# Kernel optimization log

Hardware: AMD Instinct MI355X
Metric: run time of the kernel (lower is better)

The kernel has to match this reference:

```python
import jax, jax.numpy as jnp
import numpy as np

NUT_GAIN = -0.99      # inverting nut reflection
BRIDGE_GAIN = -0.99   # inverting bridge reflection (with one-zero lowpass damping)
VIBRATE_GAIN = 0.999  # per-round-trip mute/loss gain
DISP_A = 0.7          # dispersion filter FIR blend coefficient


def _shift1(x):
    # one-sample delay along time axis: y[t] = x[t-1], y[0] = 0
    return jnp.pad(x, ((0, 0), (1, 0)))[:, :-1]


def _frac_delay(x, d):
    # fractional delay of d samples via linear interpolation: y[t] = x[t - d]
    T = x.shape[-1]
    pos = jnp.arange(T, dtype=jnp.float32) - d  # [T]
    i0 = jnp.floor(pos).astype(jnp.int32)
    f = (pos - i0).astype(x.dtype)

    def take(i):
        v = x[:, jnp.clip(i, 0, T - 1)]  # gather along time, broadcast over batch
        return jnp.where(i >= 0, v, jnp.zeros_like(v))

    return (1.0 - f) * take(i0) + f * take(i0 + 1)


def setup_inputs() -> dict:
    key = jax.random.key(0)
    k1, k2 = jax.random.split(key)
    B, T = 64, 32000  # batch_size=64, seconds=2.0 at SR=16000
    return {
        "length": 128,
        "pluckPosition": jax.random.uniform(k1, (1,), dtype=jnp.float32),
        "excitation": jax.random.normal(k2, (B, T), dtype=jnp.float32),
    }


def reference(length, pluckPosition, excitation):
    T = excitation.shape[-1]
    n_loops = T // int(length)  # matches excitation.size(-1) // int(length.min())
    p = 0.1 + 0.8 * pluckPosition[0]  # keep both string segments non-degenerate
    nUp = length * p           # nut-side segment delay (samples)
    nDown = length * (1.0 - p)  # bridge-side segment delay (samples)

    # chain._start: inject excitation into both traveling waves
    l0 = 0.5 * excitation
    r0 = 0.5 * excitation

    def step(carry, _):
        l, r, ls, rs = carry
        # _lterminate: left-going wave travels nUp to the nut and reflects
        r_next = (NUT_GAIN * VIBRATE_GAIN) * _frac_delay(l, nUp)
        # _rterminate: right-going wave through dispersion filter, nDown to bridge,
        # reflects through one-zero lowpass damping
        disp_r = DISP_A * r + (1.0 - DISP_A) * _shift1(r)
        b_in = _frac_delay(disp_r, nDown)
        l_next = (BRIDGE_GAIN * VIBRATE_GAIN * 0.5) * (b_in + _shift1(b_in))
        return (l_next, r_next, ls + l_next, rs + r_next), None

    (_, _, ls, rs), _ = jax.lax.scan(step, (l0, r0, l0, r0), None, length=n_loops)
    # torch code sums left_signal / right_signal stacks over the loop dim
    return (ls, rs)
```

## Files before the change

### kernel.cpp

```cpp
#include <hip/hip_runtime.h>


#define TLEN   32000
#define NROW   64
#define CHUNK  8000
#define NTH    1024
#define PT     16
#define PT4    (PT/4)
#define SPAN   (NTH*PT)
#define HALO   (SPAN-CHUNK)
#define PADF   1056
#define BUF    (PADF+SPAN)

__device__ inline int swz4(int f) {
  int B = f >> 2;
  B ^= (B >> 3) & 7;
  return B << 2;
}

__device__ inline float sgprf(float x) {
  return __uint_as_float(__builtin_amdgcn_readfirstlane(__float_as_uint(x)));
}

struct Cf { int DU, DD, QB; float a[2], b[4], q[5], q2[9], q4[17], q8[33]; };

__device__ inline void build_from(float Lf, float pv, Cf& c) {
  const float p   = 0.1f + 0.8f * pv;
  const float nUp = Lf * p;
  const float nDn = Lf * (1.0f - p);
  c.DU = (int)ceilf(nUp);
  c.DD = (int)ceilf(nDn);
  const float fU = (float)c.DU - nUp;
  const float fD = (float)c.DD - nDn;
  const float GN  = -0.99f * 0.999f;
  const float GB2 = -0.99f * 0.999f * 0.5f;
  c.a[0] = GN * (1.0f - fU);
  c.a[1] = GN * fU;
  const float w0 = 1.0f - fD, w1 = fD;
  c.b[0] = GB2 * (0.3f * w0);
  c.b[1] = GB2 * (w0 + 0.3f * w1);
  c.b[2] = GB2 * (0.7f * w0 + w1);
  c.b[3] = GB2 * (0.7f * w1);
  c.QB = c.DU + c.DD + 2;
#pragma unroll
  for (int m = 0; m < 5; ++m) c.q[m] = 0.f;
#pragma unroll
  for (int i = 0; i < 2; ++i)
#pragma unroll
    for (int j = 0; j < 4; ++j) c.q[i+j] = fmaf(c.a[i], c.b[j], c.q[i+j]);
#pragma unroll
  for (int m = 0; m < 9; ++m) c.q2[m] = 0.f;
#pragma unroll
  for (int i = 0; i < 5; ++i)
#pragma unroll
    for (int j = 0; j < 5; ++j) c.q2[i+j] = fmaf(c.q[i], c.q[j], c.q2[i+j]);
#pragma unroll
  for (int m = 0; m < 17; ++m) c.q4[m] = 0.f;
#pragma unroll
  for (int i = 0; i < 9; ++i)
#pragma unroll
    for (int j = 0; j < 9; ++j) c.q4[i+j] = fmaf(c.q2[i], c.q2[j], c.q4[i+j]);
#pragma unroll
  for (int m = 0; m < 33; ++m) c.q8[m] = 0.f;
#pragma unroll
  for (int i = 0; i < 17; ++i)
#pragma unroll
    for (int j = 0; j < 17; ++j) c.q8[i+j] = fmaf(c.q4[i], c.q4[j], c.q8[i+j]);
}

template<int NF4>
__device__ inline void ldwin(const float* b, int basef, float* v) {
#pragma unroll
  for (int i = 0; i < NF4; ++i) {
    float4 t4 = *(const float4*)&b[swz4(basef + 4*i)];
    v[4*i+0] = t4.x; v[4*i+1] = t4.y; v[4*i+2] = t4.z; v[4*i+3] = t4.w;
  }
}

__device__ inline void stown(float* b, const int* wro, const float* v) {
#pragma unroll
  for (int k = 0; k < PT4; ++k)
    *(float4*)&b[wro[k]] = make_float4(v[4*k], v[4*k+1], v[4*k+2], v[4*k+3]);
}

__global__ __launch_bounds__(NTH, 4)
void gs_pass(const int* __restrict__ lenp, const float* __restrict__ pp,
             const float* __restrict__ exc,
             float* __restrict__ zg, float* __restrict__ sg,
             float* __restrict__ lout, float* __restrict__ rout, int pass)
{
  __shared__ __align__(16) float bufA[BUF];
  __shared__ __align__(16) float bufB[BUF];

  const int row   = blockIdx.x >> 2;
  const int chunk = blockIdx.x & 3;
  const int t0    = chunk * CHUNK;
  const int tid   = threadIdx.x;
  const int sbase = tid * PT;
  const size_t rb = (size_t)row * TLEN;
  const int steps = pass ? 7 : 8;

  int E8;
  float W[33];
  {
    Cf c0; build_from((float)lenp[0], pp[0], c0);
#pragma unroll
    for (int m = 0; m < 33; ++m) W[m] = sgprf(c0.q8[m]);
    E8 = 8 * c0.QB;
  }

  int rdo[12], wro[PT4];
#pragma unroll
  for (int i = 0; i < 12; ++i) rdo[i] = swz4(PADF + sbase - E8 + 4*i);
#pragma unroll
  for (int k = 0; k < PT4; ++k) wro[k] = swz4(PADF + sbase + 4*k);

  const float4 f4z = make_float4(0.f, 0.f, 0.f, 0.f);
  if (tid * 4 < PADF) {
    *(float4*)&bufA[swz4(tid*4)] = f4z;
    *(float4*)&bufB[swz4(tid*4)] = f4z;
  }
  if (chunk == 0) {
    for (int s4 = tid*4; s4 < HALO; s4 += NTH*4)
      *(float4*)&bufB[swz4(PADF + s4)] = f4z;
  }
#pragma unroll
  for (int k = 0; k < 4; ++k) {
    int s4 = tid*4 + k*(NTH*4);
    int t  = t0 - HALO + s4;
    float4 v = f4z;
    if (t >= 0) {
      if (pass == 0) {
        float4 e = *(const float4*)&exc[rb + t];
        v = make_float4(0.5f*e.x, 0.5f*e.y, 0.5f*e.z, 0.5f*e.w);
      } else {
        v = *(const float4*)&zg[rb + t];
      }
    }
    *(float4*)&bufA[swz4(PADF + s4)] = v;
  }
  __syncthreads();

  float* cur = bufA;
  float* nxt = bufB;

  float z[PT], acc[PT];
#pragma unroll
  for (int k = 0; k < PT4; ++k) {
    float4 t4 = *(const float4*)&cur[wro[k]];
    z[4*k+0] = t4.x; z[4*k+1] = t4.y; z[4*k+2] = t4.z; z[4*k+3] = t4.w;
  }
#pragma unroll
  for (int j = 0; j < PT; ++j) acc[j] = 0.f;

  for (int s = 0; s < steps; ++s) {
    const int limit = (chunk == 0) ? HALO : (s + 1) * E8;
    const bool alive = (sbase + PT > limit);
    if (alive) {
      float v[48];
#pragma unroll
      for (int i = 0; i < 12; ++i) {
        float4 t4 = *(const float4*)&cur[rdo[i]];
        v[4*i+0] = t4.x; v[4*i+1] = t4.y; v[4*i+2] = t4.z; v[4*i+3] = t4.w;
      }
#pragma unroll
      for (int j = 0; j < PT; ++j) acc[j] += z[j];
#pragma unroll
      for (int j = 0; j < PT; ++j) {
        float sv = W[0] * v[j];
#pragma unroll
        for (int m = 1; m < 33; ++m) sv = fmaf(W[m], v[j+m], sv);
        z[j] = sv;
      }
      stown(nxt, wro, z);
    }
    __syncthreads();
    float* tp = cur; cur = nxt; nxt = tp;
  }

  if (pass == 0) {
    stown(nxt, wro, acc);
    __syncthreads();
#pragma unroll
    for (int k = 0; k < 2; ++k) {
      int s4 = HALO + tid*4 + k*(NTH*4);
      if (s4 < SPAN) {
        int t = t0 + s4 - HALO;
        *(float4*)&zg[rb + t] = *(const float4*)&cur[swz4(PADF + s4)];
        *(float4*)&sg[rb + t] = *(const float4*)&nxt[swz4(PADF + s4)];
      }
    }
    return;
  }

  stown(nxt, wro, acc);
  __syncthreads();
#pragma unroll
  for (int k = 0; k < 4; ++k) {
    int s4 = tid*4 + k*(NTH*4);
    int t  = t0 - HALO + s4;
    float4 sv = f4z;
    if (t >= 0) sv = *(const float4*)&sg[rb + t];
    int o = swz4(PADF + s4);
    float4 a4 = *(const float4*)&nxt[o];
    *(float4*)&nxt[o] = make_float4(a4.x + sv.x, a4.y + sv.y,
                                    a4.z + sv.z, a4.w + sv.w);
  }
  __syncthreads();

  Cf c;
  {
    volatile const int* vl = lenp;
    volatile const float* vp = pp;
    build_from((float)vl[0], vp[0], c);
  }
  const int L2 = 2*c.QB, L4 = 4*c.QB, LQ = c.QB, LB = c.DD + 2, LA = c.DU;
  const int L2e = (L2+3)&~3, sh2 = L2e-L2;
  const int LQe = (LQ+3)&~3, shq = LQe-LQ;
  const int LBe = (LB+3)&~3, shb = LBe-LB;
  const int LAe = (LA+3)&~3, sha = LAe-LA;
  float q4f[17], T2[12], TQ[8], TB[7], TA[5];
#pragma unroll
  for (int i = 0; i < 17; ++i) q4f[i] = sgprf(c.q4[i]);
#pragma unroll
  for (int m = 0; m < 12; ++m) {
    float v = 0.f;
#pragma unroll
    for (int i = 0; i < 9; ++i) if (m == sh2 + i) v = c.q2[i];
    T2[m] = sgprf(v);
  }
#pragma unroll
  for (int m = 0; m < 8; ++m) {
    float v = 0.f;
#pragma unroll
    for (int i = 0; i < 5; ++i) if (m == shq + i) v = c.q[i];
    TQ[m] = sgprf(v);
  }
#pragma unroll
  for (int m = 0; m < 7; ++m) {
    float v = 0.f;
#pragma unroll
    for (int i = 0; i < 4; ++i) if (m == shb + i) v = c.b[i];
    TB[m] = sgprf(v);
  }
#pragma unroll
  for (int m = 0; m < 5; ++m) {
    float v = 0.f;
#pragma unroll
    for (int i = 0; i < 2; ++i) if (m == sha + i) v = c.a[i];
    TA[m] = sgprf(v);
  }

  const int  F0 = 7 * E8;
  const bool ae = (chunk == 0) || (sbase + PT > F0);

  float H1[PT], Y2[PT], z62[PT];
  if (ae) {
    float e0[PT];
#pragma unroll
    for (int k = 0; k < PT4; ++k) {
      float4 t4 = *(const float4*)&nxt[wro[k]];
      e0[4*k+0] = t4.x; e0[4*k+1] = t4.y; e0[4*k+2] = t4.z; e0[4*k+3] = t4.w;
    }
    float w[28];
    ldwin<7>(nxt, PADF + sbase - L2e, w);
#pragma unroll
    for (int j = 0; j < PT; ++j) {
      float sv = e0[j];
#pragma unroll
      for (int m = 0; m < 12; ++m) sv = fmaf(T2[m], w[j+m], sv);
      H1[j] = sv;
    }
    ldwin<7>(cur, PADF + sbase - L2e, w);
#pragma unroll
    for (int j = 0; j < PT; ++j) {
      float sv = z[j];
#pragma unroll
      for (int m = 0; m < 12; ++m) sv = fmaf(T2[m], w[j+m], sv);
      Y2[j] = sv;
    }
    float w4[32];
    ldwin<8>(cur, PADF + sbase - L4, w4);
#pragma unroll
    for (int j = 0; j < PT; ++j) {
      float sv = q4f[0] * w4[j];
#pragma unroll
      for (int m = 1; m < 17; ++m) sv = fmaf(q4f[m], w4[j+m], sv);
      z62[j] = sv;
    }
  }
  __syncthreads();
  if (ae) { stown(nxt, wro, H1); stown(cur, wro, z62); }
  __syncthreads();

  float E61[PT];
  if (ae) {
    float w4[32];
    ldwin<8>(nxt, PADF + sbase - L4, w4);
#pragma unroll
    for (int j = 0; j < PT; ++j) {
      float sv = H1[j] + Y2[j];
#pragma unroll
      for (int m = 0; m < 17; ++m) sv = fmaf(q4f[m], w4[j+m], sv);
      E61[j] = sv;
    }
  }
  __syncthreads();
  if (ae) stown(nxt, wro, E61);
  __syncthreads();

  float U[PT], V[PT];
  if (ae) {
    float w[24];
    ldwin<6>(nxt, PADF + sbase - LQe, w);
#pragma unroll
    for (int j = 0; j < PT; ++j) {
      float sv = E61[j] + z62[j];
#pragma unroll
      for (int m = 0; m < 8; ++m) sv = fmaf(TQ[m], w[j+m], sv);
      U[j] = sv;
    }
    ldwin<6>(cur, PADF + sbase - LQe, w);
#pragma unroll
    for (int j = 0; j < PT; ++j) {
      float sv = TQ[0] * w[j];
#pragma unroll
      for (int m = 1; m < 8; ++m) sv = fmaf(TQ[m], w[j+m], sv);
      V[j] = sv;
    }
  }
  __syncthreads();
  if (ae) stown(nxt, wro, U);
  __syncthreads();

  float LSv[PT], RSv[PT];
  if (ae) {
#pragma unroll
    for (int j = 0; j < PT; ++j) V[j] += U[j];
    {
      float wb[24];
      ldwin<6>(nxt, PADF + sbase - LBe, wb);
#pragma unroll
      for (int j = 0; j < PT; ++j) {
        float sv = V[j];
#pragma unroll
        for (int m = 0; m < 7; ++m) sv = fmaf(TB[m], wb[j+m], sv);
        LSv[j] = sv;
      }
    }
    {
      float wa[20];
      ldwin<5>(nxt, PADF + sbase - LAe, wa);
#pragma unroll
      for (int j = 0; j < PT; ++j) {
        float sv = V[j];
#pragma unroll
        for (int m = 0; m < 5; ++m) sv = fmaf(TA[m], wa[j+m], sv);
        RSv[j] = sv;
      }
    }
  }
  __syncthreads();
  if (ae) { stown(cur, wro, LSv); stown(nxt, wro, RSv); }
  __syncthreads();

#pragma unroll
  for (int k = 0; k < 2; ++k) {
    int s4 = HALO + tid*4 + k*(NTH*4);
    if (s4 < SPAN) {
      int t = t0 + s4 - HALO;
      *(float4*)&lout[rb + t] = *(const float4*)&cur[swz4(PADF + s4)];
      *(float4*)&rout[rb + t] = *(const float4*)&nxt[swz4(PADF + s4)];
    }
  }
}

extern "C" void kernel_launch(void* const* d_in, const int* in_sizes, int n_in,
                              void* d_out, int out_size, void* d_ws, size_t ws_size,
                              hipStream_t stream) {
  (void)in_sizes; (void)n_in; (void)out_size; (void)ws_size;

  const int*   lenp = (const int*)d_in[0];
  const float* pp   = (const float*)d_in[1];
  const float* exc  = (const float*)d_in[2];

  float* lout = (float*)d_out;
  float* rout = lout + (size_t)NROW * TLEN;

  float* zg = (float*)d_ws;
  float* sg = zg + (size_t)NROW * TLEN;

  dim3 grid(NROW * 4);
  gs_pass<<<grid, dim3(NTH), 0, stream>>>(lenp, pp, exc, zg, sg, lout, rout, 0);
  gs_pass<<<grid, dim3(NTH), 0, stream>>>(lenp, pp, exc, zg, sg, lout, rout, 1);
}
```

Before: 72.04 us.

## Use 16-round composed filter in main loop and build tap tables in shared memory

Each main-loop step now advances the recursion by 16 round trips using a 65-tap filter (q16), halving the step count (4/3 instead of 8/7). An extra 8-round correction stage is added after the loop so the accumulated sum stays correct. Coefficient polynomials are now built cooperatively in shared memory instead of redundantly per thread, and global input loads are issued before the coefficient setup. The catch is a wider halo of dead work, more registers for 65 weights, and extra syncs in the setup.

```diff
diff --git a/kernel.cpp b/kernel.cpp
--- a/kernel.cpp
+++ b/kernel.cpp
@@ -21,51 +21,8 @@
 __device__ inline float sgprf(float x) {
   return __uint_as_float(__builtin_amdgcn_readfirstlane(__float_as_uint(x)));
 }
-
-struct Cf { int DU, DD, QB; float a[2], b[4], q[5], q2[9], q4[17], q8[33]; };
-
-__device__ inline void build_from(float Lf, float pv, Cf& c) {
-  const float p   = 0.1f + 0.8f * pv;
-  const float nUp = Lf * p;
-  const float nDn = Lf * (1.0f - p);
-  c.DU = (int)ceilf(nUp);
-  c.DD = (int)ceilf(nDn);
-  const float fU = (float)c.DU - nUp;
-  const float fD = (float)c.DD - nDn;
-  const float GN  = -0.99f * 0.999f;
-  const float GB2 = -0.99f * 0.999f * 0.5f;
-  c.a[0] = GN * (1.0f - fU);
-  c.a[1] = GN * fU;
-  const float w0 = 1.0f - fD, w1 = fD;
-  c.b[0] = GB2 * (0.3f * w0);
-  c.b[1] = GB2 * (w0 + 0.3f * w1);
-  c.b[2] = GB2 * (0.7f * w0 + w1);
-  c.b[3] = GB2 * (0.7f * w1);
-  c.QB = c.DU + c.DD + 2;
-#pragma unroll
-  for (int m = 0; m < 5; ++m) c.q[m] = 0.f;
-#pragma unroll
-  for (int i = 0; i < 2; ++i)
-#pragma unroll
-    for (int j = 0; j < 4; ++j) c.q[i+j] = fmaf(c.a[i], c.b[j], c.q[i+j]);
-#pragma unroll
-  for (int m = 0; m < 9; ++m) c.q2[m] = 0.f;
-#pragma unroll
-  for (int i = 0; i < 5; ++i)
-#pragma unroll
-    for (int j = 0; j < 5; ++j) c.q2[i+j] = fmaf(c.q[i], c.q[j], c.q2[i+j]);
-#pragma unroll
-  for (int m = 0; m < 17; ++m) c.q4[m] = 0.f;
-#pragma unroll
-  for (int i = 0; i < 9; ++i)
-#pragma unroll
-    for (int j = 0; j < 9; ++j) c.q4[i+j] = fmaf(c.q2[i], c.q2[j], c.q4[i+j]);
-#pragma unroll
-  for (int m = 0; m < 33; ++m) c.q8[m] = 0.f;
-#pragma unroll
-  for (int i = 0; i < 17; ++i)
-#pragma unroll
-    for (int j = 0; j < 17; ++j) c.q8[i+j] = fmaf(c.q4[i], c.q4[j], c.q8[i+j]);
+__device__ inline int sgpri(int x) {
+  return __builtin_amdgcn_readfirstlane(x);
 }
 
 template<int NF4>
@@ -91,6 +48,12 @@
 {
   __shared__ __align__(16) float bufA[BUF];
   __shared__ __align__(16) float bufB[BUF];
+  __shared__ float tq2e[25];
+  __shared__ float tq4e[49];
+  __shared__ float tq8e[97];
+  __shared__ float tq16[65];
+  __shared__ float teps[40];
+  __shared__ int   tapsI[8];
 
   const int row   = blockIdx.x >> 2;
   const int chunk = blockIdx.x & 3;
@@ -98,24 +61,97 @@
   const int tid   = threadIdx.x;
   const int sbase = tid * PT;
   const size_t rb = (size_t)row * TLEN;
-  const int steps = pass ? 7 : 8;
-
-  int E8;
-  float W[33];
-  {
-    Cf c0; build_from((float)lenp[0], pp[0], c0);
-#pragma unroll
-    for (int m = 0; m < 33; ++m) W[m] = sgprf(c0.q8[m]);
-    E8 = 8 * c0.QB;
-  }
-
-  int rdo[12], wro[PT4];
-#pragma unroll
-  for (int i = 0; i < 12; ++i) rdo[i] = swz4(PADF + sbase - E8 + 4*i);
-#pragma unroll
-  for (int k = 0; k < PT4; ++k) wro[k] = swz4(PADF + sbase + 4*k);
+  const int steps = pass ? 3 : 4;
 
   const float4 f4z = make_float4(0.f, 0.f, 0.f, 0.f);
+
+  float4 st[4];
+#pragma unroll
+  for (int k = 0; k < 4; ++k) {
+    int s4 = tid*4 + k*(NTH*4);
+    int t  = t0 - HALO + s4;
+    st[k] = f4z;
+    if (t >= 0) {
+      if (pass == 0) {
+        float4 e = *(const float4*)&exc[rb + t];
+        st[k] = make_float4(0.5f*e.x, 0.5f*e.y, 0.5f*e.z, 0.5f*e.w);
+      } else {
+        st[k] = *(const float4*)&zg[rb + t];
+      }
+    }
+  }
+
+  if (tid < 25) tq2e[tid] = 0.f;
+  if (tid < 49) tq4e[tid] = 0.f;
+  if (tid < 97) tq8e[tid] = 0.f;
+  if (tid < 40) teps[tid] = 0.f;
+  __syncthreads();
+  if (tid == 0) {
+    const float Lf  = (float)lenp[0];
+    const float p   = 0.1f + 0.8f * pp[0];
+    const float nUp = Lf * p;
+    const float nDn = Lf * (1.0f - p);
+    const int DU = (int)ceilf(nUp);
+    const int DD = (int)ceilf(nDn);
+    const float fU = (float)DU - nUp;
+    const float fD = (float)DD - nDn;
+    const float GN  = -0.99f * 0.999f;
+    const float GB2 = -0.99f * 0.999f * 0.5f;
+    const float a0 = GN * (1.0f - fU);
+    const float a1 = GN * fU;
+    const float w0 = 1.0f - fD, w1 = fD;
+    const float b0 = GB2 * (0.3f * w0);
+    const float b1 = GB2 * (w0 + 0.3f * w1);
+    const float b2 = GB2 * (0.7f * w0 + w1);
+    const float b3 = GB2 * (0.7f * w1);
+    const int QB = DU + DD + 2;
+    float q[5] = {0.f, 0.f, 0.f, 0.f, 0.f};
+    q[0] += a0*b0; q[1] += a0*b1; q[2] += a0*b2; q[3] += a0*b3;
+    q[1] += a1*b0; q[2] += a1*b1; q[3] += a1*b2; q[4] += a1*b3;
+    float q2a[9];
+#pragma unroll
+    for (int m = 0; m < 9; ++m) q2a[m] = 0.f;
+#pragma unroll
+    for (int i = 0; i < 5; ++i)
+#pragma unroll
+      for (int j = 0; j < 5; ++j) q2a[i+j] = fmaf(q[i], q[j], q2a[i+j]);
+#pragma unroll
+    for (int i = 0; i < 9; ++i) tq2e[8 + i] = q2a[i];
+    const int L2 = 2*QB, L4 = 4*QB, LQ = QB, LB = DD + 2, LA = DU;
+    const int L2e = (L2+3)&~3, LQe = (LQ+3)&~3,
+              LBe = (LB+3)&~3, LAe = (LA+3)&~3;
+#pragma unroll
+    for (int i = 0; i < 9; ++i) teps[(L2e - L2) + i] = q2a[i];
+#pragma unroll
+    for (int i = 0; i < 5; ++i) teps[16 + (LQe - LQ) + i] = q[i];
+    teps[24 + (LBe-LB) + 0] = b0; teps[24 + (LBe-LB) + 1] = b1;
+    teps[24 + (LBe-LB) + 2] = b2; teps[24 + (LBe-LB) + 3] = b3;
+    teps[32 + (LAe-LA) + 0] = a0; teps[32 + (LAe-LA) + 1] = a1;
+    tapsI[0] = 16*QB; tapsI[1] = 8*QB; tapsI[2] = L2e; tapsI[3] = L4;
+    tapsI[4] = LQe;   tapsI[5] = LBe;  tapsI[6] = LAe;
+  }
+  __syncthreads();
+  if (tid < 17) {
+    float s = 0.f;
+#pragma unroll
+    for (int i = 0; i < 9; ++i) s = fmaf(tq2e[8+i], tq2e[8 + tid - i], s);
+    tq4e[16 + tid] = s;
+  }
+  __syncthreads();
+  if (tid < 33) {
+    float s = 0.f;
+#pragma unroll
+    for (int i = 0; i < 17; ++i) s = fmaf(tq4e[16+i], tq4e[16 + tid - i], s);
+    tq8e[32 + tid] = s;
+  }
+  __syncthreads();
+  if (tid < 65) {
+    float s = 0.f;
+#pragma unroll
+    for (int i = 0; i < 33; ++i) s = fmaf(tq8e[32+i], tq8e[32 + tid - i], s);
+    tq16[tid] = s;
+  }
+
   if (tid * 4 < PADF) {
     *(float4*)&bufA[swz4(tid*4)] = f4z;
     *(float4*)&bufB[swz4(tid*4)] = f4z;
@@ -125,21 +161,20 @@
       *(float4*)&bufB[swz4(PADF + s4)] = f4z;
   }
 #pragma unroll
-  for (int k = 0; k < 4; ++k) {
-    int s4 = tid*4 + k*(NTH*4);
-    int t  = t0 - HALO + s4;
-    float4 v = f4z;
-    if (t >= 0) {
-      if (pass == 0) {
-        float4 e = *(const float4*)&exc[rb + t];
-        v = make_float4(0.5f*e.x, 0.5f*e.y, 0.5f*e.z, 0.5f*e.w);
-      } else {
-        v = *(const float4*)&zg[rb + t];
-      }
-    }
-    *(float4*)&bufA[swz4(PADF + s4)] = v;
-  }
-  __syncthreads();
+  for (int k = 0; k < 4; ++k)
+    *(float4*)&bufA[swz4(PADF + tid*4 + k*(NTH*4))] = st[k];
+  __syncthreads();
+
+  float W16[65];
+#pragma unroll
+  for (int m = 0; m < 65; ++m) W16[m] = sgprf(tq16[m]);
+  const int E16 = sgpri(tapsI[0]);
+
+  int rdoD[20], wro[PT4];
+#pragma unroll
+  for (int i = 0; i < 20; ++i) rdoD[i] = swz4(PADF + sbase - E16 + 4*i);
+#pragma unroll
+  for (int k = 0; k < PT4; ++k) wro[k] = swz4(PADF + sbase + 4*k);
 
   float* cur = bufA;
   float* nxt = bufB;
@@ -154,24 +189,37 @@
   for (int j = 0; j < PT; ++j) acc[j] = 0.f;
 
   for (int s = 0; s < steps; ++s) {
-    const int limit = (chunk == 0) ? HALO : (s + 1) * E8;
-    const bool alive = (sbase + PT > limit);
-    if (alive) {
-      float v[48];
-#pragma unroll
-      for (int i = 0; i < 12; ++i) {
-        float4 t4 = *(const float4*)&cur[rdo[i]];
-        v[4*i+0] = t4.x; v[4*i+1] = t4.y; v[4*i+2] = t4.z; v[4*i+3] = t4.w;
+    const int wlim = (chunk == 0) ? HALO : (s + 1) * E16;
+    const int alim = (chunk == 0) ? HALO : (pass ? s * E16 : wlim);
+    if (sbase + PT > alim) {
+#pragma unroll
+      for (int j = 0; j < PT; ++j) acc[j] += z[j];
+    }
+    if (sbase + PT > wlim) {
+      float nz[PT];
+#pragma unroll
+      for (int j = 0; j < PT; ++j) nz[j] = 0.f;
+#pragma unroll
+      for (int c = 0; c < 5; ++c) {
+        float vv[16];
+#pragma unroll
+        for (int i = 0; i < 4; ++i) {
+          float4 t4 = *(const float4*)&cur[rdoD[4*c + i]];
+          vv[4*i+0] = t4.x; vv[4*i+1] = t4.y;
+          vv[4*i+2] = t4.z; vv[4*i+3] = t4.w;
+        }
+#pragma unroll
+        for (int mi = 0; mi < 16; ++mi) {
+          const int idx = 16*c + mi;
+#pragma unroll
+          for (int j = 0; j < PT; ++j) {
+            const int m = idx - j;
+            if (m >= 0 && m < 65) nz[j] = fmaf(W16[m], vv[mi], nz[j]);
+          }
+        }
       }
 #pragma unroll
-      for (int j = 0; j < PT; ++j) acc[j] += z[j];
-#pragma unroll
-      for (int j = 0; j < PT; ++j) {
-        float sv = W[0] * v[j];
-#pragma unroll
-        for (int m = 1; m < 33; ++m) sv = fmaf(W[m], v[j+m], sv);
-        z[j] = sv;
-      }
+      for (int j = 0; j < PT; ++j) z[j] = nz[j];
       stown(nxt, wro, z);
     }
     __syncthreads();
@@ -195,64 +243,90 @@
 
   stown(nxt, wro, acc);
   __syncthreads();
-#pragma unroll
-  for (int k = 0; k < 4; ++k) {
-    int s4 = tid*4 + k*(NTH*4);
-    int t  = t0 - HALO + s4;
-    float4 sv = f4z;
-    if (t >= 0) sv = *(const float4*)&sg[rb + t];
-    int o = swz4(PADF + s4);
-    float4 a4 = *(const float4*)&nxt[o];
-    *(float4*)&nxt[o] = make_float4(a4.x + sv.x, a4.y + sv.y,
-                                    a4.z + sv.z, a4.w + sv.w);
-  }
-  __syncthreads();
-
-  Cf c;
   {
-    volatile const int* vl = lenp;
-    volatile const float* vp = pp;
-    build_from((float)vl[0], vp[0], c);
-  }
-  const int L2 = 2*c.QB, L4 = 4*c.QB, LQ = c.QB, LB = c.DD + 2, LA = c.DU;
-  const int L2e = (L2+3)&~3, sh2 = L2e-L2;
-  const int LQe = (LQ+3)&~3, shq = LQe-LQ;
-  const int LBe = (LB+3)&~3, shb = LBe-LB;
-  const int LAe = (LA+3)&~3, sha = LAe-LA;
+    const int SG_LO = 3 * E16 - 64;
+#pragma unroll
+    for (int k = 0; k < 4; ++k) {
+      int s4 = tid*4 + k*(NTH*4);
+      int t  = t0 - HALO + s4;
+      float4 sv = f4z;
+      if (t >= 0 && (chunk == 0 || s4 >= SG_LO))
+        sv = *(const float4*)&sg[rb + t];
+      int o = swz4(PADF + s4);
+      float4 a4 = *(const float4*)&nxt[o];
+      *(float4*)&nxt[o] = make_float4(a4.x + sv.x, a4.y + sv.y,
+                                      a4.z + sv.z, a4.w + sv.w);
+    }
+  }
+  __syncthreads();
+  asm volatile("" ::: "memory");
+  float W8[33];
+#pragma unroll
+  for (int m = 0; m < 33; ++m) W8[m] = sgprf(tq8e[32 + m]);
+  const int E8 = sgpri(tapsI[1]);
+  const int F0 = 7 * E8;
+  const bool ae = (chunk == 0) || (sbase + PT > F0);
+  float E14[PT], Y15[PT];
+  if (ae) {
+    int rdo8[12];
+#pragma unroll
+    for (int i = 0; i < 12; ++i) rdo8[i] = swz4(PADF + sbase - E8 + 4*i);
+    float g0[PT];
+#pragma unroll
+    for (int k = 0; k < PT4; ++k) {
+      float4 t4 = *(const float4*)&nxt[wro[k]];
+      g0[4*k+0] = t4.x; g0[4*k+1] = t4.y; g0[4*k+2] = t4.z; g0[4*k+3] = t4.w;
+    }
+    float v[48];
+#pragma unroll
+    for (int i = 0; i < 12; ++i) {
+      float4 t4 = *(const float4*)&nxt[rdo8[i]];
+      v[4*i+0] = t4.x; v[4*i+1] = t4.y; v[4*i+2] = t4.z; v[4*i+3] = t4.w;
+    }
+#pragma unroll
+    for (int j = 0; j < PT; ++j) {
+      float sv = g0[j] + z[j];
+#pragma unroll
+      for (int m = 0; m < 33; ++m) sv = fmaf(W8[m], v[j+m], sv);
+      E14[j] = sv;
+    }
+#pragma unroll
+    for (int i = 0; i < 12; ++i) {
+      float4 t4 = *(const float4*)&cur[rdo8[i]];
+      v[4*i+0] = t4.x; v[4*i+1] = t4.y; v[4*i+2] = t4.z; v[4*i+3] = t4.w;
+    }
+#pragma unroll
+    for (int j = 0; j < PT; ++j) {
+      float sv = W8[0] * v[j];
+#pragma unroll
+      for (int m = 1; m < 33; ++m) sv = fmaf(W8[m], v[j+m], sv);
+      Y15[j] = sv;
+    }
+  }
+  __syncthreads();
+  if (ae) {
+    stown(nxt, wro, E14);
+    stown(cur, wro, Y15);
+#pragma unroll
+    for (int j = 0; j < PT; ++j) z[j] = Y15[j];
+  }
+  __syncthreads();
+
+  asm volatile("" ::: "memory");
   float q4f[17], T2[12], TQ[8], TB[7], TA[5];
 #pragma unroll
-  for (int i = 0; i < 17; ++i) q4f[i] = sgprf(c.q4[i]);
-#pragma unroll
-  for (int m = 0; m < 12; ++m) {
-    float v = 0.f;
-#pragma unroll
-    for (int i = 0; i < 9; ++i) if (m == sh2 + i) v = c.q2[i];
-    T2[m] = sgprf(v);
-  }
-#pragma unroll
-  for (int m = 0; m < 8; ++m) {
-    float v = 0.f;
-#pragma unroll
-    for (int i = 0; i < 5; ++i) if (m == shq + i) v = c.q[i];
-    TQ[m] = sgprf(v);
-  }
-#pragma unroll
-  for (int m = 0; m < 7; ++m) {
-    float v = 0.f;
-#pragma unroll
-    for (int i = 0; i < 4; ++i) if (m == shb + i) v = c.b[i];
-    TB[m] = sgprf(v);
-  }
-#pragma unroll
-  for (int m = 0; m < 5; ++m) {
-    float v = 0.f;
-#pragma unroll
-    for (int i = 0; i < 2; ++i) if (m == sha + i) v = c.a[i];
-    TA[m] = sgprf(v);
-  }
-
-  const int  F0 = 7 * E8;
-  const bool ae = (chunk == 0) || (sbase + PT > F0);
+  for (int i = 0; i < 17; ++i) q4f[i] = sgprf(tq4e[16 + i]);
+#pragma unroll
+  for (int m = 0; m < 12; ++m) T2[m] = sgprf(teps[m]);
+#pragma unroll
+  for (int m = 0; m < 8; ++m) TQ[m] = sgprf(teps[16 + m]);
+#pragma unroll
+  for (int m = 0; m < 7; ++m) TB[m] = sgprf(teps[24 + m]);
+#pragma unroll
+  for (int m = 0; m < 5; ++m) TA[m] = sgprf(teps[32 + m]);
+  const int L2e = sgpri(tapsI[2]), L4  = sgpri(tapsI[3]),
+            LQe = sgpri(tapsI[4]), LBe = sgpri(tapsI[5]),
+            LAe = sgpri(tapsI[6]);
 
   float H1[PT], Y2[PT], z62[PT];
   if (ae) {
@@ -391,6 +465,8 @@
   float* sg = zg + (size_t)NROW * TLEN;
 
   dim3 grid(NROW * 4);
-  gs_pass<<<grid, dim3(NTH), 0, stream>>>(lenp, pp, exc, zg, sg, lout, rout, 0);
-  gs_pass<<<grid, dim3(NTH), 0, stream>>>(lenp, pp, exc, zg, sg, lout, rout, 1);
-}
+  gs_pass<<<grid, dim3(NTH), 0, stream>>>(lenp, pp, exc, zg, sg,
+                                          lout, rout, 0);
+  gs_pass<<<grid, dim3(NTH), 0, stream>>>(lenp, pp, exc, zg, sg,
+                                          lout, rout, 1);
+}
```

Result: slower. 81.27 us (+12.8%).

## Replace per-step block barriers with neighbor-wave LDS flag synchronization

Applied to the files above, without the earlier changes.

Each stencil step in the main loop used to end in a block-wide __syncthreads. It now uses per-wave progress and read-done flags in LDS. Each wave spins only on the two waves whose data it reads and on the two that read its output, so waves can drift apart instead of all waiting on the slowest. Separately, the pass-1 global load of sg is skipped for regions outside the active window. This adds spin-polling overhead and relies on correct LDS memory ordering across waves; if the flag dependencies are wrong it risks races or deadlock.

```diff
diff --git a/kernel.cpp b/kernel.cpp
--- a/kernel.cpp
+++ b/kernel.cpp
@@ -5,6 +5,7 @@
 #define NROW   64
 #define CHUNK  8000
 #define NTH    1024
+#define NWV    (NTH/64)
 #define PT     16
 #define PT4    (PT/4)
 #define SPAN   (NTH*PT)
@@ -20,6 +21,12 @@
 
 __device__ inline float sgprf(float x) {
   return __uint_as_float(__builtin_amdgcn_readfirstlane(__float_as_uint(x)));
+}
+
+__device__ inline void spinge(const int* f, int v) {
+  while (((const volatile int*)f)[0] < v) __builtin_amdgcn_s_sleep(1);
+  asm volatile("" ::: "memory");
+  __builtin_amdgcn_sched_barrier(0);
 }
 
 struct Cf { int DU, DD, QB; float a[2], b[4], q[5], q2[9], q4[17], q8[33]; };
@@ -91,6 +98,8 @@
 {
   __shared__ __align__(16) float bufA[BUF];
   __shared__ __align__(16) float bufB[BUF];
+  __shared__ int progF[NWV];
+  __shared__ int rdpF[NWV];
 
   const int row   = blockIdx.x >> 2;
   const int chunk = blockIdx.x & 3;
@@ -99,6 +108,10 @@
   const int sbase = tid * PT;
   const size_t rb = (size_t)row * TLEN;
   const int steps = pass ? 7 : 8;
+  const int w     = tid >> 6;
+  const int wtop  = ((w + 1) << 6) * PT;
+
+  if (tid < NWV) { progF[tid] = 0; rdpF[tid] = 0; }
 
   int E8;
   float W[33];
@@ -155,28 +168,48 @@
 
   for (int s = 0; s < steps; ++s) {
     const int limit = (chunk == 0) ? HALO : (s + 1) * E8;
-    const bool alive = (sbase + PT > limit);
-    if (alive) {
+    const bool walive = (wtop > limit);
+    const bool alive  = (sbase + PT > limit);
+    if (walive) {
+      if (s > 0) {
+        if (w >= 1) spinge(&progF[w-1], s);
+        if (w >= 2) spinge(&progF[w-2], s);
+      }
       float v[48];
-#pragma unroll
-      for (int i = 0; i < 12; ++i) {
-        float4 t4 = *(const float4*)&cur[rdo[i]];
-        v[4*i+0] = t4.x; v[4*i+1] = t4.y; v[4*i+2] = t4.z; v[4*i+3] = t4.w;
-      }
-#pragma unroll
-      for (int j = 0; j < PT; ++j) acc[j] += z[j];
-#pragma unroll
-      for (int j = 0; j < PT; ++j) {
-        float sv = W[0] * v[j];
-#pragma unroll
-        for (int m = 1; m < 33; ++m) sv = fmaf(W[m], v[j+m], sv);
-        z[j] = sv;
-      }
-      stown(nxt, wro, z);
-    }
-    __syncthreads();
+      if (alive) {
+#pragma unroll
+        for (int i = 0; i < 12; ++i) {
+          float4 t4 = *(const float4*)&cur[rdo[i]];
+          v[4*i+0] = t4.x; v[4*i+1] = t4.y; v[4*i+2] = t4.z; v[4*i+3] = t4.w;
+        }
+      }
+      asm volatile("s_waitcnt lgkmcnt(0)" ::: "memory");
+      if ((tid & 63) == 0) ((volatile int*)rdpF)[w] = s + 1;
+      if (alive) {
+#pragma unroll
+        for (int j = 0; j < PT; ++j) acc[j] += z[j];
+#pragma unroll
+        for (int j = 0; j < PT; ++j) {
+          float sv = W[0] * v[j];
+#pragma unroll
+          for (int m = 1; m < 33; ++m) sv = fmaf(W[m], v[j+m], sv);
+          z[j] = sv;
+        }
+      }
+      if (w + 1 < NWV) spinge(&rdpF[w+1], s);
+      if (w + 2 < NWV) spinge(&rdpF[w+2], s);
+      if (alive) stown(nxt, wro, z);
+      asm volatile("s_waitcnt lgkmcnt(0)" ::: "memory");
+      if ((tid & 63) == 0) ((volatile int*)progF)[w] = s + 1;
+    } else {
+      if ((tid & 63) == 0) {
+        ((volatile int*)rdpF)[w]  = s + 1;
+        ((volatile int*)progF)[w] = s + 1;
+      }
+    }
     float* tp = cur; cur = nxt; nxt = tp;
   }
+  __syncthreads();
 
   if (pass == 0) {
     stown(nxt, wro, acc);
@@ -193,6 +226,7 @@
     return;
   }
 
+  const int F0 = 7 * E8;
   stown(nxt, wro, acc);
   __syncthreads();
 #pragma unroll
@@ -200,7 +234,8 @@
     int s4 = tid*4 + k*(NTH*4);
     int t  = t0 - HALO + s4;
     float4 sv = f4z;
-    if (t >= 0) sv = *(const float4*)&sg[rb + t];
+    if (t >= 0 && (chunk == 0 || s4 >= F0 - 600))
+      sv = *(const float4*)&sg[rb + t];
     int o = swz4(PADF + s4);
     float4 a4 = *(const float4*)&nxt[o];
     *(float4*)&nxt[o] = make_float4(a4.x + sv.x, a4.y + sv.y,
@@ -251,7 +286,6 @@
     TA[m] = sgprf(v);
   }
 
-  const int  F0 = 7 * E8;
   const bool ae = (chunk == 0) || (sbase + PT > F0);
 
   float H1[PT], Y2[PT], z62[PT];
@@ -262,21 +296,21 @@
       float4 t4 = *(const float4*)&nxt[wro[k]];
       e0[4*k+0] = t4.x; e0[4*k+1] = t4.y; e0[4*k+2] = t4.z; e0[4*k+3] = t4.w;
     }
-    float w[28];
-    ldwin<7>(nxt, PADF + sbase - L2e, w);
+    float wv[28];
+    ldwin<7>(nxt, PADF + sbase - L2e, wv);
 #pragma unroll
     for (int j = 0; j < PT; ++j) {
       float sv = e0[j];
 #pragma unroll
-      for (int m = 0; m < 12; ++m) sv = fmaf(T2[m], w[j+m], sv);
+      for (int m = 0; m < 12; ++m) sv = fmaf(T2[m], wv[j+m], sv);
       H1[j] = sv;
     }
-    ldwin<7>(cur, PADF + sbase - L2e, w);
+    ldwin<7>(cur, PADF + sbase - L2e, wv);
 #pragma unroll
     for (int j = 0; j < PT; ++j) {
       float sv = z[j];
 #pragma unroll
-      for (int m = 0; m < 12; ++m) sv = fmaf(T2[m], w[j+m], sv);
+      for (int m = 0; m < 12; ++m) sv = fmaf(T2[m], wv[j+m], sv);
       Y2[j] = sv;
     }
     float w4[32];
@@ -311,21 +345,21 @@
 
   float U[PT], V[PT];
   if (ae) {
-    float w[24];
-    ldwin<6>(nxt, PADF + sbase - LQe, w);
+    float wv[24];
+    ldwin<6>(nxt, PADF + sbase - LQe, wv);
 #pragma unroll
     for (int j = 0; j < PT; ++j) {
       float sv = E61[j] + z62[j];
 #pragma unroll
-      for (int m = 0; m < 8; ++m) sv = fmaf(TQ[m], w[j+m], sv);
+      for (int m = 0; m < 8; ++m) sv = fmaf(TQ[m], wv[j+m], sv);
       U[j] = sv;
     }
-    ldwin<6>(cur, PADF + sbase - LQe, w);
-#pragma unroll
-    for (int j = 0; j < PT; ++j) {
-      float sv = TQ[0] * w[j];
-#pragma unroll
-      for (int m = 1; m < 8; ++m) sv = fmaf(TQ[m], w[j+m], sv);
+    ldwin<6>(cur, PADF + sbase - LQe, wv);
+#pragma unroll
+    for (int j = 0; j < PT; ++j) {
+      float sv = TQ[0] * wv[j];
+#pragma unroll
+      for (int m = 1; m < 8; ++m) sv = fmaf(TQ[m], wv[j+m], sv);
       V[j] = sv;
     }
   }
```

Measured after the change: 122.4 us. 69.9% more time.
